# Optimization experiments

Measured on AMD Instinct MI355X. Metric: run time of the kernel, lower is better.

Reference implementation:

```python
import jax, jax.numpy as jnp
import numpy as np

N, C, L, E, H = 2000, 4, 5000, 64000, 512
REP = 207  # length after conv front-end: floor((floor((5000-11)/4)+1 - 11)/6)+1


def setup_inputs() -> dict:
    key = jax.random.key(0)
    ks = jax.random.split(key, 10)

    def init(k, shape, fan_in):
        return jax.random.normal(k, shape, jnp.float32) / np.sqrt(fan_in).astype(np.float32)

    x = jax.random.normal(ks[0], (N, C, L), jnp.float32)
    edge_index = jax.random.randint(ks[1], (2, E), 0, N)
    return dict(
        x=x, edge_index=edge_index,
        w1=init(ks[2], (16, C, 1), C), b1=jnp.zeros(16, jnp.float32),
        w2=init(ks[3], (4, 4, 11), 4 * 11), b2=jnp.zeros(4, jnp.float32),
        w3=init(ks[4], (1, 4, 11), 4 * 11), b3=jnp.zeros(1, jnp.float32),
        gcn_w=init(ks[5], (REP, H), REP), gcn_b=jnp.zeros(H, jnp.float32),
        lin_w=init(ks[6], (REP, H), REP), lin_b=jnp.zeros(H, jnp.float32),
        gate_w=init(ks[7], (H, H), H), gate_b=jnp.zeros(H, jnp.float32),
        bn_gamma=jnp.ones(H, jnp.float32), bn_beta=jnp.zeros(H, jnp.float32),
    )


def _conv1d(x, w, b, stride):
    # x: [N, Cin, L], w: [Cout, Cin, K] (torch OIH layout), VALID padding
    y = jax.lax.conv_general_dilated(x, w, (stride,), 'VALID',
                                     dimension_numbers=('NCH', 'OIH', 'NCH'))
    return y + b[None, :, None]


def _gcn_conv(feat, edge_index, w, b, n):
    # GCNConv: x@W, add self-loops, sym-normalize, scatter-add, + bias
    h = feat @ w                                      # [N, H]
    loops = jnp.arange(n)
    src = jnp.concatenate([edge_index[0], loops])
    dst = jnp.concatenate([edge_index[1], loops])
    deg = jax.ops.segment_sum(jnp.ones_like(src, h.dtype), dst, num_segments=n)
    dinv = jax.lax.rsqrt(deg)                         # deg >= 1 due to self-loops
    norm = dinv[src] * dinv[dst]                      # [E+N]
    out = jax.ops.segment_sum(h[src] * norm[:, None], dst, num_segments=n)
    return out + b


def reference(x, edge_index, w1, b1, w2, b2, w3, b3,
              gcn_w, gcn_b, lin_w, lin_b, gate_w, gate_b, bn_gamma, bn_beta):
    n = x.shape[0]
    # conv front-end (dropout layers are identity at inference)
    h = jax.nn.relu(_conv1d(x, w1, b1, 1))            # [N, 16, L]
    # MaxPool1d(k=4,s=4) applied on permuted [N, L, 16] == pool over channel dim
    h = h.reshape(n, 4, 4, L).max(axis=2)             # [N, 4, L]
    h = jax.nn.relu(_conv1d(h, w2, b2, 4))            # [N, 4, 1248]
    h = jax.nn.relu(_conv1d(h, w3, b3, 6))            # [N, 1, 207]
    feat = h[:, 0, :]                                 # squeeze -> [N, REP]
    # GCN + gated fusion
    z = jnp.tanh(_gcn_conv(feat, edge_index, gcn_w, gcn_b, n))
    g = jax.nn.sigmoid(z @ gate_w + gate_b)
    xl = feat @ lin_w + lin_b
    out = jax.nn.relu((1.0 - g) * xl + g * z)
    # BatchNorm over node dim (batch statistics, training-mode semantics)
    mean = out.mean(axis=0)
    var = out.var(axis=0)
    out = (out - mean) * jax.lax.rsqrt(var + 1e-5) * bn_gamma + bn_beta
    return out
```

## Files before the change

kernel.cpp:

```cpp
#include <hip/hip_runtime.h>
#include <hip/hip_bf16.h>
#include <cstddef>

#define NN 2000
#define CC 4
#define LL1 5000
#define LL2 1248
#define LL3 207
#define FSTR 208
#define HH 512
#define EE 64000

__device__ float g_feat[NN * FSTR];
__device__ float g_aggf[NN * FSTR];
__device__ float g_z[NN * HH];
__device__ float g_xl[NN * HH];
__device__ float g_obuf[NN * HH];
__device__ float g_dinv[NN];
__device__ float g_colsum[HH];
__device__ float g_colsq[HH];
__device__ int   g_cnt[NN];
__device__ int   g_cursor[NN];
__device__ int   g_off[NN];
__device__ int   g_bucket[EE];

__global__ void zero_init() {
    int i = blockIdx.x * 256 + threadIdx.x;
    if (i < NN) { g_cnt[i] = 0; g_cursor[i] = 0; }
    if (i < HH) { g_colsum[i] = 0.f; g_colsq[i] = 0.f; }
}

#define MCH 1256
__global__ __launch_bounds__(256) void conv_chain(
    const float* __restrict__ x,
    const float* __restrict__ w1, const float* __restrict__ b1,
    const float* __restrict__ w2, const float* __restrict__ b2,
    const float* __restrict__ w3, const float* __restrict__ b3)
{
    __shared__ __align__(16) float sm[4 * MCH];
    __shared__ __align__(16) float sy[4 * LL2];

    const int tid = threadIdx.x;
    const int node = blockIdx.x;
    const float* xb = x + (size_t)node * (CC * LL1);

    float w1r[64], b1r[16];
#pragma unroll
    for (int i = 0; i < 64; ++i) w1r[i] = w1[i];
#pragma unroll
    for (int i = 0; i < 16; ++i) b1r[i] = b1[i];

#pragma unroll 1
    for (int c = 0; c < 4; ++c) {
        const int l0 = 1248 * c;
        for (int g4 = tid; g4 < 314; g4 += 256) {
            const int l = l0 + 4 * g4;
            float xs[4][4];
#pragma unroll
            for (int ch = 0; ch < 4; ++ch)
                *(float4*)xs[ch] = *(const float4*)(xb + ch * LL1 + l);
#pragma unroll
            for (int g = 0; g < 4; ++g) {
                float mv[4];
#pragma unroll
                for (int li = 0; li < 4; ++li) {
                    float best = -1e30f;
#pragma unroll
                    for (int j = 0; j < 4; ++j) {
                        int o = g * 4 + j;
                        float v = b1r[o] + w1r[o*4+0]*xs[0][li] + w1r[o*4+1]*xs[1][li]
                                         + w1r[o*4+2]*xs[2][li] + w1r[o*4+3]*xs[3][li];
                        best = fmaxf(best, v);
                    }
                    mv[li] = fmaxf(best, 0.f);
                }
                *(float4*)&sm[g * MCH + 4 * g4] = make_float4(mv[0], mv[1], mv[2], mv[3]);
            }
        }
        __syncthreads();

        const int T0 = 312 * c;
#pragma unroll 1
        for (int pair = 0; pair < 2; ++pair) {
            const float* wp = w2 + 88 * pair;
            float wo[88];
#pragma unroll
            for (int i = 0; i < 88; ++i) wo[i] = wp[i];
            const float bo0 = b2[2 * pair], bo1 = b2[2 * pair + 1];
            for (int T = tid; T < 312; T += 256) {
                float a0 = bo0, a1 = bo1;
#pragma unroll
                for (int i = 0; i < 4; ++i) {
                    const float* mp = sm + i * MCH + 4 * T;
                    float4 u0 = *(const float4*)mp;
                    float4 u1 = *(const float4*)(mp + 4);
                    float4 u2 = *(const float4*)(mp + 8);
                    float v[12] = {u0.x, u0.y, u0.z, u0.w,
                                   u1.x, u1.y, u1.z, u1.w,
                                   u2.x, u2.y, u2.z, u2.w};
#pragma unroll
                    for (int k = 0; k < 11; ++k) {
                        a0 += wo[i * 11 + k] * v[k];
                        a1 += wo[44 + i * 11 + k] * v[k];
                    }
                }
                sy[(2 * pair) * LL2 + T0 + T]     = fmaxf(a0, 0.f);
                sy[(2 * pair + 1) * LL2 + T0 + T] = fmaxf(a1, 0.f);
            }
        }
        __syncthreads();
    }

    if (tid < FSTR) {
        float acc = 0.f;
        if (tid < LL3) {
            acc = b3[0];
#pragma unroll
            for (int i = 0; i < 4; ++i)
#pragma unroll
                for (int k = 0; k < 11; ++k)
                    acc += w3[i * 11 + k] * sy[i * LL2 + 6 * tid + k];
            acc = fmaxf(acc, 0.f);
        }
        g_feat[(size_t)node * FSTR + tid] = acc;
    }
}

__global__ void edge_count(const int* __restrict__ ei, int E) {
    int e = blockIdx.x * 256 + threadIdx.x;
    if (e < E) atomicAdd(&g_cnt[ei[E + e]], 1);
}

__global__ __launch_bounds__(256) void scan_dinv() {
    __shared__ int a[2048], b[2048];
    int tid = threadIdx.x;
    for (int i = tid; i < 2048; i += 256) a[i] = (i < NN) ? g_cnt[i] : 0;
    __syncthreads();
    int* src = a; int* dst = b;
    for (int d = 1; d < 2048; d <<= 1) {
        for (int i = tid; i < 2048; i += 256)
            dst[i] = src[i] + ((i >= d) ? src[i - d] : 0);
        __syncthreads();
        int* t = src; src = dst; dst = t;
    }
    for (int i = tid; i < NN; i += 256) {
        g_off[i] = src[i] - g_cnt[i];
        g_dinv[i] = rsqrtf(1.0f + (float)g_cnt[i]);
    }
}

__global__ void bucket_fill(const int* __restrict__ ei, int E) {
    int e = blockIdx.x * 256 + threadIdx.x;
    if (e < E) {
        int d = ei[E + e];
        int p = atomicAdd(&g_cursor[d], 1);
        g_bucket[g_off[d] + p] = ei[e];
    }
}

__global__ __launch_bounds__(256) void agg_feat() {
    const int sub = threadIdx.x >> 6;
    const int lane = threadIdx.x & 63;
    const int d = blockIdx.x * 4 + sub;
    if (lane >= 52) return;
    const float di = g_dinv[d];
    const int nb = g_cnt[d];
    const int base = g_off[d];
    const size_t co = (size_t)lane * 4;
    float4 a = *(const float4*)(g_feat + (size_t)d * FSTR + co);
    float ax = a.x * di, ay = a.y * di, az = a.z * di, aw = a.w * di;
    int j = 0;
    for (; j + 1 < nb; j += 2) {
        int s0 = g_bucket[base + j];
        int s1 = g_bucket[base + j + 1];
        float w0 = g_dinv[s0], w1 = g_dinv[s1];
        float4 f0 = *(const float4*)(g_feat + (size_t)s0 * FSTR + co);
        float4 f1 = *(const float4*)(g_feat + (size_t)s1 * FSTR + co);
        ax += f0.x * w0 + f1.x * w1;
        ay += f0.y * w0 + f1.y * w1;
        az += f0.z * w0 + f1.z * w1;
        aw += f0.w * w0 + f1.w * w1;
    }
    if (j < nb) {
        int s = g_bucket[base + j];
        float w = g_dinv[s];
        float4 f = *(const float4*)(g_feat + (size_t)s * FSTR + co);
        ax += f.x * w; ay += f.y * w; az += f.z * w; aw += f.w * w;
    }
    *(float4*)(g_aggf + (size_t)d * FSTR + co) = make_float4(ax * di, ay * di, az * di, aw * di);
}

__global__ __launch_bounds__(256) void gemm_zxl(
    const float* __restrict__ gcn_w, const float* __restrict__ gcn_b,
    const float* __restrict__ lin_w, const float* __restrict__ lin_b)
{
    __shared__ float As[2][16][33];
    __shared__ float Bs[2][16][32];
    const int tid = threadIdx.x;
    const int which = blockIdx.z;
    const float* __restrict__ A = which ? g_feat : g_aggf;
    const float* __restrict__ B = which ? lin_w : gcn_w;
    const float* __restrict__ bias = which ? lin_b : gcn_b;
    float* __restrict__ C = which ? g_xl : g_z;
    const int N0 = blockIdx.x * 32, M0 = blockIdx.y * 32;
    const int lr = tid >> 4, lk = tid & 15;
    const int bk = tid >> 4, bn = (tid & 15) * 2;
    const int ty = tid >> 3, tx = tid & 7;

    float acc[4] = {0.f, 0.f, 0.f, 0.f};
    float ra0, ra1; float2 rbv;
    const int r0 = M0 + lr, r1 = M0 + lr + 16;

    ra0 = (r0 < NN) ? A[(size_t)r0 * FSTR + lk] : 0.f;
    ra1 = (r1 < NN) ? A[(size_t)r1 * FSTR + lk] : 0.f;
    rbv = (bk < LL3) ? *(const float2*)(B + (size_t)bk * HH + N0 + bn) : make_float2(0.f, 0.f);
    As[0][lk][lr] = ra0; As[0][lk][lr + 16] = ra1;
    Bs[0][bk][bn] = rbv.x; Bs[0][bk][bn + 1] = rbv.y;
    __syncthreads();

#pragma unroll 1
    for (int kt = 0; kt < 13; ++kt) {
        const int cur = kt & 1;
        if (kt + 1 < 13) {
            int k0 = (kt + 1) * 16;
            ra0 = (r0 < NN) ? A[(size_t)r0 * FSTR + k0 + lk] : 0.f;
            ra1 = (r1 < NN) ? A[(size_t)r1 * FSTR + k0 + lk] : 0.f;
            int kb = k0 + bk;
            rbv = (kb < LL3) ? *(const float2*)(B + (size_t)kb * HH + N0 + bn) : make_float2(0.f, 0.f);
        }
#pragma unroll
        for (int k = 0; k < 16; ++k) {
            float av = As[cur][k][ty];
            float4 b4 = *(const float4*)&Bs[cur][k][tx * 4];
            acc[0] += av * b4.x; acc[1] += av * b4.y; acc[2] += av * b4.z; acc[3] += av * b4.w;
        }
        if (kt + 1 < 13) {
            const int nxt = cur ^ 1;
            As[nxt][lk][lr] = ra0; As[nxt][lk][lr + 16] = ra1;
            Bs[nxt][bk][bn] = rbv.x; Bs[nxt][bk][bn + 1] = rbv.y;
        }
        __syncthreads();
    }

    const int r = M0 + ty;
    if (r < NN) {
        const int c0 = N0 + tx * 4;
        float4 bb = *(const float4*)(bias + c0);
        float4 v = make_float4(acc[0] + bb.x, acc[1] + bb.y, acc[2] + bb.z, acc[3] + bb.w);
        if (which == 0) { v.x = tanhf(v.x); v.y = tanhf(v.y); v.z = tanhf(v.z); v.w = tanhf(v.w); }
        *(float4*)(C + (size_t)r * HH + c0) = v;
    }
}

__global__ __launch_bounds__(256) void gemm_gate(
    const float* __restrict__ gate_w, const float* __restrict__ gate_b)
{
    __shared__ float As[2][16][33];
    __shared__ float Bs[2][16][32];
    __shared__ float rs[32], rq[32];
    const int tid = threadIdx.x;
    const float* __restrict__ A = g_z;
    const int N0 = blockIdx.x * 32, M0 = blockIdx.y * 32;
    const int lr = tid >> 4, lk = tid & 15;
    const int bk = tid >> 4, bn = (tid & 15) * 2;
    const int ty = tid >> 3, tx = tid & 7;

    float acc[4] = {0.f, 0.f, 0.f, 0.f};
    float ra0, ra1; float2 rbv;
    const int r0 = M0 + lr, r1 = M0 + lr + 16;

    ra0 = (r0 < NN) ? A[(size_t)r0 * HH + lk] : 0.f;
    ra1 = (r1 < NN) ? A[(size_t)r1 * HH + lk] : 0.f;
    rbv = *(const float2*)(gate_w + (size_t)bk * HH + N0 + bn);
    As[0][lk][lr] = ra0; As[0][lk][lr + 16] = ra1;
    Bs[0][bk][bn] = rbv.x; Bs[0][bk][bn + 1] = rbv.y;
    __syncthreads();

#pragma unroll 1
    for (int kt = 0; kt < 32; ++kt) {
        const int cur = kt & 1;
        if (kt + 1 < 32) {
            int k0 = (kt + 1) * 16;
            ra0 = (r0 < NN) ? A[(size_t)r0 * HH + k0 + lk] : 0.f;
            ra1 = (r1 < NN) ? A[(size_t)r1 * HH + k0 + lk] : 0.f;
            rbv = *(const float2*)(gate_w + (size_t)(k0 + bk) * HH + N0 + bn);
        }
#pragma unroll
        for (int k = 0; k < 16; ++k) {
            float av = As[cur][k][ty];
            float4 b4 = *(const float4*)&Bs[cur][k][tx * 4];
            acc[0] += av * b4.x; acc[1] += av * b4.y; acc[2] += av * b4.z; acc[3] += av * b4.w;
        }
        if (kt + 1 < 32) {
            const int nxt = cur ^ 1;
            As[nxt][lk][lr] = ra0; As[nxt][lk][lr + 16] = ra1;
            Bs[nxt][bk][bn] = rbv.x; Bs[nxt][bk][bn + 1] = rbv.y;
        }
        __syncthreads();
    }

    const int r = M0 + ty;
    const int c0 = N0 + tx * 4;
    float cs[4] = {0.f, 0.f, 0.f, 0.f}, cq[4] = {0.f, 0.f, 0.f, 0.f};
    if (r < NN) {
        float4 bb = *(const float4*)(gate_b + c0);
        float4 xv = *(const float4*)(g_xl + (size_t)r * HH + c0);
        float4 zv = *(const float4*)(g_z + (size_t)r * HH + c0);
        float pre[4] = {acc[0] + bb.x, acc[1] + bb.y, acc[2] + bb.z, acc[3] + bb.w};
        float xa[4] = {xv.x, xv.y, xv.z, xv.w};
        float za[4] = {zv.x, zv.y, zv.z, zv.w};
        float va[4];
#pragma unroll
        for (int j = 0; j < 4; ++j) {
            float g = 1.f / (1.f + __expf(-pre[j]));
            float v = fmaxf((1.f - g) * xa[j] + g * za[j], 0.f);
            va[j] = v; cs[j] = v; cq[j] = v * v;
        }
        *(float4*)(g_obuf + (size_t)r * HH + c0) = make_float4(va[0], va[1], va[2], va[3]);
    }
    if (tid < 32) { rs[tid] = 0.f; rq[tid] = 0.f; }
    __syncthreads();
#pragma unroll
    for (int j = 0; j < 4; ++j) {
        atomicAdd(&rs[tx * 4 + j], cs[j]);
        atomicAdd(&rq[tx * 4 + j], cq[j]);
    }
    __syncthreads();
    if (tid < 32) {
        atomicAdd(&g_colsum[N0 + tid], rs[tid]);
        atomicAdd(&g_colsq[N0 + tid], rq[tid]);
    }
}

__global__ __launch_bounds__(256) void bn_apply(const float* __restrict__ gamma,
                                                const float* __restrict__ beta,
                                                float* __restrict__ out) {
    int i = blockIdx.x * 256 + threadIdx.x;
    int c = i & (HH - 1);
    float mean = g_colsum[c] * (1.f / (float)NN);
    float var = g_colsq[c] * (1.f / (float)NN) - mean * mean;
    float s = rsqrtf(var + 1e-5f) * gamma[c];
    out[i] = g_obuf[i] * s + (beta[c] - mean * s);
}

extern "C" void kernel_launch(void* const* d_in, const int* in_sizes, int n_in,
                              void* d_out, int out_size, void* d_ws, size_t ws_size,
                              hipStream_t stream) {
    (void)d_ws; (void)ws_size; (void)n_in; (void)out_size;
    const float* x      = (const float*)d_in[0];
    const int*   ei     = (const int*)d_in[1];
    const float* w1     = (const float*)d_in[2];
    const float* b1     = (const float*)d_in[3];
    const float* w2     = (const float*)d_in[4];
    const float* b2     = (const float*)d_in[5];
    const float* w3     = (const float*)d_in[6];
    const float* b3     = (const float*)d_in[7];
    const float* gcn_w  = (const float*)d_in[8];
    const float* gcn_b  = (const float*)d_in[9];
    const float* lin_w  = (const float*)d_in[10];
    const float* lin_b  = (const float*)d_in[11];
    const float* gate_w = (const float*)d_in[12];
    const float* gate_b = (const float*)d_in[13];
    const float* bn_g   = (const float*)d_in[14];
    const float* bn_b   = (const float*)d_in[15];
    float* out = (float*)d_out;
    const int E = in_sizes[1] / 2;

    zero_init<<<8, 256, 0, stream>>>();
    conv_chain<<<NN, 256, 0, stream>>>(x, w1, b1, w2, b2, w3, b3);
    edge_count<<<(E + 255) / 256, 256, 0, stream>>>(ei, E);
    scan_dinv<<<1, 256, 0, stream>>>();
    bucket_fill<<<(E + 255) / 256, 256, 0, stream>>>(ei, E);
    agg_feat<<<NN / 4, 256, 0, stream>>>();

    gemm_zxl<<<dim3(HH / 32, (NN + 31) / 32, 2), 256, 0, stream>>>(gcn_w, gcn_b, lin_w, lin_b);
    gemm_gate<<<dim3(HH / 32, (NN + 31) / 32), 256, 0, stream>>>(gate_w, gate_b);

    bn_apply<<<(NN * HH) / 256, 256, 0, stream>>>(bn_g, bn_b, out);
}
```

Before: 384.9 us.

## Enlarge GEMM tiles to 64x64 with 4x4 register blocking; fold zero-init into conv

Both dense GEMM kernels move from 32x32 tiles with 1x4 outputs per thread to 64x64 tiles with a 4x4 register micro-tile and float4 global and shared loads. This raises arithmetic intensity per shared-memory read and reduces redundant global traffic. The gate GEMM epilogue now accumulates column statistics over four rows per thread before the atomics. Separately, the zero_init launch is removed and its work is done by the first 8 blocks of conv_chain, saving one kernel launch. The larger tiles produce fewer blocks (256 for the gate GEMM), which may underfill the GPU's compute units.

```diff
diff --git a/kernel.cpp b/kernel.cpp
--- a/kernel.cpp
+++ b/kernel.cpp
@@ -24,12 +24,6 @@
 __device__ int   g_off[NN];
 __device__ int   g_bucket[EE];
 
-__global__ void zero_init() {
-    int i = blockIdx.x * 256 + threadIdx.x;
-    if (i < NN) { g_cnt[i] = 0; g_cursor[i] = 0; }
-    if (i < HH) { g_colsum[i] = 0.f; g_colsq[i] = 0.f; }
-}
-
 #define MCH 1256
 __global__ __launch_bounds__(256) void conv_chain(
     const float* __restrict__ x,
@@ -42,6 +36,13 @@
 
     const int tid = threadIdx.x;
     const int node = blockIdx.x;
+
+    if (node < 8) {
+        int i = node * 256 + tid;
+        if (i < NN) { g_cnt[i] = 0; g_cursor[i] = 0; }
+        if (i < HH) { g_colsum[i] = 0.f; g_colsq[i] = 0.f; }
+    }
+
     const float* xb = x + (size_t)node * (CC * LL1);
 
     float w1r[64], b1r[16];
@@ -194,131 +195,157 @@
     const float* __restrict__ gcn_w, const float* __restrict__ gcn_b,
     const float* __restrict__ lin_w, const float* __restrict__ lin_b)
 {
-    __shared__ float As[2][16][33];
-    __shared__ float Bs[2][16][32];
+    __shared__ __align__(16) float As[2][16][68];
+    __shared__ __align__(16) float Bs[2][16][68];
     const int tid = threadIdx.x;
     const int which = blockIdx.z;
     const float* __restrict__ A = which ? g_feat : g_aggf;
     const float* __restrict__ B = which ? lin_w : gcn_w;
     const float* __restrict__ bias = which ? lin_b : gcn_b;
     float* __restrict__ C = which ? g_xl : g_z;
-    const int N0 = blockIdx.x * 32, M0 = blockIdx.y * 32;
-    const int lr = tid >> 4, lk = tid & 15;
-    const int bk = tid >> 4, bn = (tid & 15) * 2;
-    const int ty = tid >> 3, tx = tid & 7;
-
-    float acc[4] = {0.f, 0.f, 0.f, 0.f};
-    float ra0, ra1; float2 rbv;
-    const int r0 = M0 + lr, r1 = M0 + lr + 16;
-
-    ra0 = (r0 < NN) ? A[(size_t)r0 * FSTR + lk] : 0.f;
-    ra1 = (r1 < NN) ? A[(size_t)r1 * FSTR + lk] : 0.f;
-    rbv = (bk < LL3) ? *(const float2*)(B + (size_t)bk * HH + N0 + bn) : make_float2(0.f, 0.f);
-    As[0][lk][lr] = ra0; As[0][lk][lr + 16] = ra1;
-    Bs[0][bk][bn] = rbv.x; Bs[0][bk][bn + 1] = rbv.y;
+    const int N0 = blockIdx.x * 64, M0 = blockIdx.y * 64;
+    const int ar = tid >> 2, ak = (tid & 3) * 4;
+    const int bk = tid >> 4, bn = (tid & 15) * 4;
+    const int ty = tid >> 4, tx = tid & 15;
+    const int rowA = M0 + ar;
+
+    float acc[16];
+#pragma unroll
+    for (int i = 0; i < 16; ++i) acc[i] = 0.f;
+    const float4 z4 = make_float4(0.f, 0.f, 0.f, 0.f);
+    float4 rA, rB;
+
+    rA = (rowA < NN) ? *(const float4*)(A + (size_t)rowA * FSTR + ak) : z4;
+    rB = (bk < LL3) ? *(const float4*)(B + (size_t)bk * HH + N0 + bn) : z4;
+    As[0][ak+0][ar] = rA.x; As[0][ak+1][ar] = rA.y;
+    As[0][ak+2][ar] = rA.z; As[0][ak+3][ar] = rA.w;
+    *(float4*)&Bs[0][bk][bn] = rB;
     __syncthreads();
 
 #pragma unroll 1
     for (int kt = 0; kt < 13; ++kt) {
         const int cur = kt & 1;
         if (kt + 1 < 13) {
-            int k0 = (kt + 1) * 16;
-            ra0 = (r0 < NN) ? A[(size_t)r0 * FSTR + k0 + lk] : 0.f;
-            ra1 = (r1 < NN) ? A[(size_t)r1 * FSTR + k0 + lk] : 0.f;
-            int kb = k0 + bk;
-            rbv = (kb < LL3) ? *(const float2*)(B + (size_t)kb * HH + N0 + bn) : make_float2(0.f, 0.f);
+            const int k0 = (kt + 1) * 16;
+            rA = (rowA < NN) ? *(const float4*)(A + (size_t)rowA * FSTR + k0 + ak) : z4;
+            const int kb = k0 + bk;
+            rB = (kb < LL3) ? *(const float4*)(B + (size_t)kb * HH + N0 + bn) : z4;
         }
 #pragma unroll
         for (int k = 0; k < 16; ++k) {
-            float av = As[cur][k][ty];
-            float4 b4 = *(const float4*)&Bs[cur][k][tx * 4];
-            acc[0] += av * b4.x; acc[1] += av * b4.y; acc[2] += av * b4.z; acc[3] += av * b4.w;
+            const float4 a4 = *(const float4*)&As[cur][k][ty * 4];
+            const float4 b4 = *(const float4*)&Bs[cur][k][tx * 4];
+            const float av[4] = {a4.x, a4.y, a4.z, a4.w};
+            const float bv[4] = {b4.x, b4.y, b4.z, b4.w};
+#pragma unroll
+            for (int i = 0; i < 4; ++i)
+#pragma unroll
+                for (int j = 0; j < 4; ++j)
+                    acc[i * 4 + j] += av[i] * bv[j];
         }
         if (kt + 1 < 13) {
             const int nxt = cur ^ 1;
-            As[nxt][lk][lr] = ra0; As[nxt][lk][lr + 16] = ra1;
-            Bs[nxt][bk][bn] = rbv.x; Bs[nxt][bk][bn + 1] = rbv.y;
+            As[nxt][ak+0][ar] = rA.x; As[nxt][ak+1][ar] = rA.y;
+            As[nxt][ak+2][ar] = rA.z; As[nxt][ak+3][ar] = rA.w;
+            *(float4*)&Bs[nxt][bk][bn] = rB;
         }
         __syncthreads();
     }
 
-    const int r = M0 + ty;
-    if (r < NN) {
-        const int c0 = N0 + tx * 4;
-        float4 bb = *(const float4*)(bias + c0);
-        float4 v = make_float4(acc[0] + bb.x, acc[1] + bb.y, acc[2] + bb.z, acc[3] + bb.w);
-        if (which == 0) { v.x = tanhf(v.x); v.y = tanhf(v.y); v.z = tanhf(v.z); v.w = tanhf(v.w); }
-        *(float4*)(C + (size_t)r * HH + c0) = v;
+    const int c0 = N0 + tx * 4;
+    const float4 bb = *(const float4*)(bias + c0);
+#pragma unroll
+    for (int i = 0; i < 4; ++i) {
+        const int r = M0 + ty * 4 + i;
+        if (r < NN) {
+            float4 v = make_float4(acc[i*4+0] + bb.x, acc[i*4+1] + bb.y,
+                                   acc[i*4+2] + bb.z, acc[i*4+3] + bb.w);
+            if (which == 0) { v.x = tanhf(v.x); v.y = tanhf(v.y); v.z = tanhf(v.z); v.w = tanhf(v.w); }
+            *(float4*)(C + (size_t)r * HH + c0) = v;
+        }
     }
 }
 
 __global__ __launch_bounds__(256) void gemm_gate(
     const float* __restrict__ gate_w, const float* __restrict__ gate_b)
 {
-    __shared__ float As[2][16][33];
-    __shared__ float Bs[2][16][32];
-    __shared__ float rs[32], rq[32];
+    __shared__ __align__(16) float As[2][16][68];
+    __shared__ __align__(16) float Bs[2][16][68];
+    __shared__ float rs[64], rq[64];
     const int tid = threadIdx.x;
     const float* __restrict__ A = g_z;
-    const int N0 = blockIdx.x * 32, M0 = blockIdx.y * 32;
-    const int lr = tid >> 4, lk = tid & 15;
-    const int bk = tid >> 4, bn = (tid & 15) * 2;
-    const int ty = tid >> 3, tx = tid & 7;
-
-    float acc[4] = {0.f, 0.f, 0.f, 0.f};
-    float ra0, ra1; float2 rbv;
-    const int r0 = M0 + lr, r1 = M0 + lr + 16;
-
-    ra0 = (r0 < NN) ? A[(size_t)r0 * HH + lk] : 0.f;
-    ra1 = (r1 < NN) ? A[(size_t)r1 * HH + lk] : 0.f;
-    rbv = *(const float2*)(gate_w + (size_t)bk * HH + N0 + bn);
-    As[0][lk][lr] = ra0; As[0][lk][lr + 16] = ra1;
-    Bs[0][bk][bn] = rbv.x; Bs[0][bk][bn + 1] = rbv.y;
+    const int N0 = blockIdx.x * 64, M0 = blockIdx.y * 64;
+    const int ar = tid >> 2, ak = (tid & 3) * 4;
+    const int bk = tid >> 4, bn = (tid & 15) * 4;
+    const int ty = tid >> 4, tx = tid & 15;
+    const int rowA = M0 + ar;
+
+    float acc[16];
+#pragma unroll
+    for (int i = 0; i < 16; ++i) acc[i] = 0.f;
+    const float4 z4 = make_float4(0.f, 0.f, 0.f, 0.f);
+    float4 rA, rB;
+
+    rA = (rowA < NN) ? *(const float4*)(A + (size_t)rowA * HH + ak) : z4;
+    rB = *(const float4*)(gate_w + (size_t)bk * HH + N0 + bn);
+    As[0][ak+0][ar] = rA.x; As[0][ak+1][ar] = rA.y;
+    As[0][ak+2][ar] = rA.z; As[0][ak+3][ar] = rA.w;
+    *(float4*)&Bs[0][bk][bn] = rB;
     __syncthreads();
 
 #pragma unroll 1
     for (int kt = 0; kt < 32; ++kt) {
         const int cur = kt & 1;
         if (kt + 1 < 32) {
-            int k0 = (kt + 1) * 16;
-            ra0 = (r0 < NN) ? A[(size_t)r0 * HH + k0 + lk] : 0.f;
-            ra1 = (r1 < NN) ? A[(size_t)r1 * HH + k0 + lk] : 0.f;
-            rbv = *(const float2*)(gate_w + (size_t)(k0 + bk) * HH + N0 + bn);
+            const int k0 = (kt + 1) * 16;
+            rA = (rowA < NN) ? *(const float4*)(A + (size_t)rowA * HH + k0 + ak) : z4;
+            rB = *(const float4*)(gate_w + (size_t)(k0 + bk) * HH + N0 + bn);
         }
 #pragma unroll
         for (int k = 0; k < 16; ++k) {
-            float av = As[cur][k][ty];
-            float4 b4 = *(const float4*)&Bs[cur][k][tx * 4];
-            acc[0] += av * b4.x; acc[1] += av * b4.y; acc[2] += av * b4.z; acc[3] += av * b4.w;
+            const float4 a4 = *(const float4*)&As[cur][k][ty * 4];
+            const float4 b4 = *(const float4*)&Bs[cur][k][tx * 4];
+            const float av[4] = {a4.x, a4.y, a4.z, a4.w};
+            const float bv[4] = {b4.x, b4.y, b4.z, b4.w};
+#pragma unroll
+            for (int i = 0; i < 4; ++i)
+#pragma unroll
+                for (int j = 0; j < 4; ++j)
+                    acc[i * 4 + j] += av[i] * bv[j];
         }
         if (kt + 1 < 32) {
             const int nxt = cur ^ 1;
-            As[nxt][lk][lr] = ra0; As[nxt][lk][lr + 16] = ra1;
-            Bs[nxt][bk][bn] = rbv.x; Bs[nxt][bk][bn + 1] = rbv.y;
+            As[nxt][ak+0][ar] = rA.x; As[nxt][ak+1][ar] = rA.y;
+            As[nxt][ak+2][ar] = rA.z; As[nxt][ak+3][ar] = rA.w;
+            *(float4*)&Bs[nxt][bk][bn] = rB;
         }
         __syncthreads();
     }
 
-    const int r = M0 + ty;
     const int c0 = N0 + tx * 4;
+    const float4 bb = *(const float4*)(gate_b + c0);
     float cs[4] = {0.f, 0.f, 0.f, 0.f}, cq[4] = {0.f, 0.f, 0.f, 0.f};
-    if (r < NN) {
-        float4 bb = *(const float4*)(gate_b + c0);
-        float4 xv = *(const float4*)(g_xl + (size_t)r * HH + c0);
-        float4 zv = *(const float4*)(g_z + (size_t)r * HH + c0);
-        float pre[4] = {acc[0] + bb.x, acc[1] + bb.y, acc[2] + bb.z, acc[3] + bb.w};
-        float xa[4] = {xv.x, xv.y, xv.z, xv.w};
-        float za[4] = {zv.x, zv.y, zv.z, zv.w};
-        float va[4];
-#pragma unroll
-        for (int j = 0; j < 4; ++j) {
-            float g = 1.f / (1.f + __expf(-pre[j]));
-            float v = fmaxf((1.f - g) * xa[j] + g * za[j], 0.f);
-            va[j] = v; cs[j] = v; cq[j] = v * v;
-        }
-        *(float4*)(g_obuf + (size_t)r * HH + c0) = make_float4(va[0], va[1], va[2], va[3]);
-    }
-    if (tid < 32) { rs[tid] = 0.f; rq[tid] = 0.f; }
+#pragma unroll
+    for (int i = 0; i < 4; ++i) {
+        const int r = M0 + ty * 4 + i;
+        if (r < NN) {
+            const float4 xv = *(const float4*)(g_xl + (size_t)r * HH + c0);
+            const float4 zv = *(const float4*)(g_z + (size_t)r * HH + c0);
+            const float pre[4] = {acc[i*4+0] + bb.x, acc[i*4+1] + bb.y,
+                                  acc[i*4+2] + bb.z, acc[i*4+3] + bb.w};
+            const float xa[4] = {xv.x, xv.y, xv.z, xv.w};
+            const float za[4] = {zv.x, zv.y, zv.z, zv.w};
+            float va[4];
+#pragma unroll
+            for (int j = 0; j < 4; ++j) {
+                float g = 1.f / (1.f + __expf(-pre[j]));
+                float v = fmaxf((1.f - g) * xa[j] + g * za[j], 0.f);
+                va[j] = v; cs[j] += v; cq[j] += v * v;
+            }
+            *(float4*)(g_obuf + (size_t)r * HH + c0) = make_float4(va[0], va[1], va[2], va[3]);
+        }
+    }
+    if (tid < 64) { rs[tid] = 0.f; rq[tid] = 0.f; }
     __syncthreads();
 #pragma unroll
     for (int j = 0; j < 4; ++j) {
@@ -326,7 +353,7 @@
         atomicAdd(&rq[tx * 4 + j], cq[j]);
     }
     __syncthreads();
-    if (tid < 32) {
+    if (tid < 64) {
         atomicAdd(&g_colsum[N0 + tid], rs[tid]);
         atomicAdd(&g_colsq[N0 + tid], rq[tid]);
     }
@@ -366,15 +393,14 @@
     float* out = (float*)d_out;
     const int E = in_sizes[1] / 2;
 
-    zero_init<<<8, 256, 0, stream>>>();
     conv_chain<<<NN, 256, 0, stream>>>(x, w1, b1, w2, b2, w3, b3);
     edge_count<<<(E + 255) / 256, 256, 0, stream>>>(ei, E);
     scan_dinv<<<1, 256, 0, stream>>>();
     bucket_fill<<<(E + 255) / 256, 256, 0, stream>>>(ei, E);
     agg_feat<<<NN / 4, 256, 0, stream>>>();
 
-    gemm_zxl<<<dim3(HH / 32, (NN + 31) / 32, 2), 256, 0, stream>>>(gcn_w, gcn_b, lin_w, lin_b);
-    gemm_gate<<<dim3(HH / 32, (NN + 31) / 32), 256, 0, stream>>>(gate_w, gate_b);
+    gemm_zxl<<<dim3(HH / 64, (NN + 63) / 64, 2), 256, 0, stream>>>(gcn_w, gcn_b, lin_w, lin_b);
+    gemm_gate<<<dim3(HH / 64, (NN + 63) / 64), 256, 0, stream>>>(gate_w, gate_b);
 
     bn_apply<<<(NN * HH) / 256, 256, 0, stream>>>(bn_g, bn_b, out);
 }
```

Measured after the change: 367.4 us. -4.6%, faster.
